# Optimization experiments

Measured on AMD Instinct MI355X. Metric: run time of the kernel, lower is better.

## Reference

```python
import jax, jax.numpy as jnp
import numpy as np

L, N, K, S, V, H = 12, 2048, 8, 4, 50000, 256


def setup_inputs() -> dict:
    key = jax.random.key(0)
    ks = jax.random.split(key, 20)
    tokens1 = jax.random.randint(ks[0], (L, N, S), 0, V, dtype=jnp.int32)
    tokens2 = jax.random.randint(ks[1], (L, N, S), 0, V, dtype=jnp.int32)
    # child indices into previous level's h (0 = zero-init row, -1 = no child)
    idx1 = jax.random.randint(ks[2], (L, N, K), -1, N + 1, dtype=jnp.int32).at[0].set(-1)
    idx2 = jax.random.randint(ks[3], (L, N, K), -1, N + 1, dtype=jnp.int32).at[0].set(-1)
    sc = 0.02
    E = jax.random.normal(ks[4], (V, H), jnp.float32)  # torch.randn init
    lin_W = jax.random.normal(ks[5], (H * S, H), jnp.float32) * sc
    lin_b = jnp.zeros((H,), jnp.float32)
    Uf_W = jax.random.normal(ks[6], (H, H), jnp.float32) * sc
    Uf_b = jnp.zeros((H,), jnp.float32)
    Uiuo_W = jax.random.normal(ks[7], (H, 3 * H), jnp.float32) * sc
    Uiuo_b = jnp.zeros((3 * H,), jnp.float32)
    W_W = jax.random.normal(ks[8], (H, 4 * H), jnp.float32) * sc
    W_b = jnp.zeros((4 * H,), jnp.float32)
    dense_W = jax.random.normal(ks[9], (H, 512), jnp.float32) * sc
    dense_b = jnp.zeros((512,), jnp.float32)
    out_W = jax.random.normal(ks[10], (512, 2), jnp.float32) * sc
    out_b = jnp.zeros((2,), jnp.float32)
    return dict(tokens1=tokens1, idx1=idx1, tokens2=tokens2, idx2=idx2,
                E=E, lin_W=lin_W, lin_b=lin_b, Uf_W=Uf_W, Uf_b=Uf_b,
                Uiuo_W=Uiuo_W, Uiuo_b=Uiuo_b, W_W=W_W, W_b=W_b,
                dense_W=dense_W, dense_b=dense_b, out_W=out_W, out_b=out_b)


def _encode(tokens, idx, E, lin_W, lin_b, Uf_W, Uf_b, Uiuo_W, Uiuo_b, W_W, W_b):
    # TreeEmbeddingLayer: lookup label_size tokens per node, concat, linear
    emb = E[tokens].reshape(L, N, S * H)           # [L,N,S*H]
    x = emb @ lin_W + lin_b                        # [L,N,H]

    def step(carry, inp):
        h_prev, c_prev = carry                     # [N,H]
        xl, il = inp                               # [N,H], [N,K]
        zero = jnp.zeros((1, H), xl.dtype)
        hp = jnp.concatenate([zero, h_prev], 0)    # [N+1,H] (row 0 = init)
        cp = jnp.concatenate([zero, c_prev], 0)
        mask_bool = il != -1
        index = jnp.where(mask_bool, il, 0)
        h = hp[index]                              # [N,K,H] gather child states
        c = cp[index]
        m = mask_bool[..., None].astype(xl.dtype)  # [N,K,1]
        h_sum = jnp.sum(h * m, axis=1)             # [N,H]
        Wx = xl @ W_W + W_b                        # [N,4H]
        Wf, Wi, Wu, Wo = Wx[:, :H], Wx[:, H:2*H], Wx[:, 2*H:3*H], Wx[:, 3*H:]
        fk = jax.nn.sigmoid(Wf[:, None, :] + h @ Uf_W + Uf_b)  # [N,K,H]
        bf = jnp.sum(fk * c * m, axis=1)           # [N,H]
        iuo = h_sum @ Uiuo_W + Uiuo_b              # [N,3H]
        i = jax.nn.sigmoid(iuo[:, :H] + Wi)
        u = jnp.tanh(iuo[:, H:2*H] + Wu)
        o = jax.nn.sigmoid(iuo[:, 2*H:] + Wo)
        nc = i * u + bf
        nh = o * jnp.tanh(nc)
        return (nh, nc), nh

    init = (jnp.zeros((N, H), x.dtype), jnp.zeros((N, H), x.dtype))
    (_, _), hs = jax.lax.scan(step, init, (x, idx))
    # 1 layer with skip connection; hx = last (root) level
    return hs[-1] + x[-1]                          # [N,H]


def reference(tokens1, idx1, tokens2, idx2, E, lin_W, lin_b, Uf_W, Uf_b,
              Uiuo_W, Uiuo_b, W_W, W_b, dense_W, dense_b, out_W, out_b):
    h1 = _encode(tokens1, idx1, E, lin_W, lin_b, Uf_W, Uf_b, Uiuo_W, Uiuo_b, W_W, W_b)
    h2 = _encode(tokens2, idx2, E, lin_W, lin_b, Uf_W, Uf_b, Uiuo_W, Uiuo_b, W_W, W_b)
    abs_dist = jnp.abs(h1 - h2)                    # [N,H]
    x = jnp.tanh(abs_dist @ dense_W + dense_b)     # dropout = identity (eval)
    logits = x @ out_W + out_b                     # [N,2]
    return jax.nn.softmax(logits, axis=-1)
```

## Files before the change

### kernel.cpp

```cpp
#include <hip/hip_runtime.h>

#define LL 12
#define NN 2048
#define KK 8
#define SS 4
#define HH 256
#define LN (LL*NN)
#define VV 50000
#define ZROW 4096
#define SROW 1536

typedef __bf16 bf16_t;
typedef __bf16 bf16x8 __attribute__((ext_vector_type(8)));
typedef __bf16 bf16x4v __attribute__((ext_vector_type(4)));
typedef float f32x4 __attribute__((ext_vector_type(4)));

__device__ __forceinline__ float sigmoidf_(float x) { return 1.f / (1.f + expf(-x)); }

__global__ __launch_bounds__(256) void k_cvtE(const float* __restrict__ src,
                                              bf16_t* __restrict__ dst, int n4)
{
    int i = blockIdx.x * 256 + threadIdx.x;
    const int stride = gridDim.x * 256;
    for (; i < n4; i += stride) {
        const float4 v = ((const float4*)src)[i];
        bf16x4v o;
        o[0] = (bf16_t)v.x; o[1] = (bf16_t)v.y; o[2] = (bf16_t)v.z; o[3] = (bf16_t)v.w;
        ((bf16x4v*)dst)[i] = o;
    }
}

__global__ __launch_bounds__(256) void k_cvtW(
    const float* __restrict__ linW, const float* __restrict__ WW,
    const float* __restrict__ UfW, const float* __restrict__ UiW,
    bf16_t* __restrict__ linWt, bf16_t* __restrict__ WWt,
    bf16_t* __restrict__ UfWt, bf16_t* __restrict__ UiWt)
{
    int i = blockIdx.x * 256 + threadIdx.x;
    if (i < 262144) {
        const int rr = i >> 8, cc = i & 255;
        linWt[(size_t)cc * 1024 + rr] = (bf16_t)linW[i];
        return;
    }
    i -= 262144;
    if (i < 262144) {
        const int rr = i >> 10, cc = i & 1023;
        WWt[(size_t)cc * 256 + rr] = (bf16_t)WW[i];
        return;
    }
    i -= 262144;
    if (i < 65536) {
        const int rr = i >> 8, cc = i & 255;
        UfWt[(size_t)cc * 256 + rr] = (bf16_t)UfW[i];
        return;
    }
    i -= 65536;
    if (i < 196608) {
        const int rr = i / 768, cc = i - rr * 768;
        UiWt[(size_t)cc * 256 + rr] = (bf16_t)UiW[i];
    }
}

__global__ __launch_bounds__(256) void k_zero(float* __restrict__ SA, float* __restrict__ SB)
{
    const int t = threadIdx.x;
    float* a = SA + (size_t)ZROW * 384;
    float* b = SB + (size_t)ZROW * 384;
    for (int i = t; i < 384; i += 256) { a[i] = 0.f; b[i] = 0.f; }
}

__global__ __launch_bounds__(256) void k_embed(
    const int* __restrict__ tok1, const int* __restrict__ tok2,
    const bf16_t* __restrict__ Ebf, const bf16_t* __restrict__ linWt,
    const float* __restrict__ linb, bf16_t* __restrict__ xout)
{
    __shared__ int toff[64][SS];
    const int t = threadIdx.x;
    const int m0 = blockIdx.x * 64;
    {
        const int lr = t >> 2, s = t & 3;
        const int m = m0 + lr;
        const int e = (m >= LN) ? 1 : 0;
        const int rrow = m - e * LN;
        const int* tok = e ? tok2 : tok1;
        toff[lr][s] = tok[(size_t)rrow * SS + s] * HH;
    }
    __syncthreads();
    const int lane = t & 63, w = t >> 6;
    const int wm = w >> 1, wn = w & 1;
    const int r = lane & 15, kg = lane >> 4;
    const int lr0 = wm * 32 + r, lr1 = lr0 + 16;
    const bf16_t* bp[8];
    #pragma unroll
    for (int j = 0; j < 8; ++j)
        bp[j] = linWt + (size_t)(wn * 128 + j * 16 + r) * 1024 + kg * 8;

    const f32x4 zero = {0.f, 0.f, 0.f, 0.f};
    f32x4 acc[2][8];
    #pragma unroll
    for (int mi = 0; mi < 2; ++mi)
        #pragma unroll
        for (int j = 0; j < 8; ++j) acc[mi][j] = zero;

    for (int k0 = 0; k0 < 1024; k0 += 32) {
        const int s = k0 >> 8, off = (k0 & 255) + kg * 8;
        const bf16x8 a0 = *(const bf16x8*)(Ebf + (size_t)toff[lr0][s] + off);
        const bf16x8 a1 = *(const bf16x8*)(Ebf + (size_t)toff[lr1][s] + off);
        #pragma unroll
        for (int j = 0; j < 8; ++j) {
            const bf16x8 b = *(const bf16x8*)bp[j];
            acc[0][j] = __builtin_amdgcn_mfma_f32_16x16x32_bf16(a0, b, acc[0][j], 0, 0, 0);
            acc[1][j] = __builtin_amdgcn_mfma_f32_16x16x32_bf16(a1, b, acc[1][j], 0, 0, 0);
            bp[j] += 32;
        }
    }
    const int crow = m0 + wm * 32 + kg * 4;
    #pragma unroll
    for (int j = 0; j < 8; ++j) {
        const int ccol = wn * 128 + j * 16 + r;
        const float bv = linb[ccol];
        #pragma unroll
        for (int mi = 0; mi < 2; ++mi)
            #pragma unroll
            for (int jj = 0; jj < 4; ++jj)
                xout[(size_t)(crow + mi * 16 + jj) * HH + ccol] =
                    (bf16_t)(acc[mi][j][jj] + bv);
    }
}

__global__ __launch_bounds__(512, 2) void k_step(
    const bf16_t* __restrict__ xbf,
    const int* __restrict__ idx1, const int* __restrict__ idx2, const int l,
    const bf16_t* __restrict__ UfWt, const float* __restrict__ Ufb,
    const bf16_t* __restrict__ UiWt, const float* __restrict__ Uib,
    const bf16_t* __restrict__ WWt, const float* __restrict__ Wb,
    const char* __restrict__ Sprev, char* __restrict__ Snext)
{
    __shared__ __align__(16) bf16_t WxL[16 * 1024];
    __shared__ __align__(16) bf16_t iuoL[16 * 768];
    __shared__ __align__(16) bf16_t hsumL[16 * 256];

    const int t = threadIdx.x;
    const int bid = blockIdx.x;
    const int x  = bid & 7;
    const int e  = x >> 2;
    const int n0 = ((bid >> 3) * 4 + (x & 3)) * 16;
    const int g0 = e * NN + n0;
    const int lane = t & 63, w = t >> 6;
    const int r = lane & 15, kg = lane >> 4;
    const f32x4 zero = {0.f, 0.f, 0.f, 0.f};

    const int rr = t >> 5, sl = t & 31;
    const int ss = (sl + 4 * (rr & 7)) & 31;

    int ch[KK];
    {
        const int* idxp = (e ? idx2 : idx1) + ((size_t)l * NN + n0 + rr) * KK;
        const int4 i0 = *(const int4*)idxp;
        const int4 i1 = *(const int4*)(idxp + 4);
        ch[0] = i0.x; ch[1] = i0.y; ch[2] = i0.z; ch[3] = i0.w;
        ch[4] = i1.x; ch[5] = i1.y; ch[6] = i1.z; ch[7] = i1.w;
        #pragma unroll
        for (int k = 0; k < KK; ++k)
            ch[k] = (ch[k] >= 1) ? (e * NN + ch[k] - 1) : ZROW;
    }

    bf16x8 hv[KK];
    #pragma unroll
    for (int k = 0; k < KK; ++k)
        hv[k] = *(const bf16x8*)(Sprev + (size_t)ch[k] * SROW + sl * 16);

    const bf16_t* xrow = xbf + ((size_t)e * LN + (size_t)l * NN + n0 + r) * HH + kg * 8;
    bf16x8 aWx[8];
    #pragma unroll
    for (int k = 0; k < 8; ++k) aWx[k] = *(const bf16x8*)(xrow + k * 32);

    {
        const bf16_t* bw[8];
        #pragma unroll
        for (int j = 0; j < 8; ++j)
            bw[j] = WWt + (size_t)((8 * w + j) * 16 + r) * HH + kg * 8;
        f32x4 acc[8];
        #pragma unroll
        for (int j = 0; j < 8; ++j) acc[j] = zero;
        #pragma unroll
        for (int k = 0; k < 8; ++k) {
            #pragma unroll
            for (int j = 0; j < 8; ++j) {
                const bf16x8 b = *(const bf16x8*)bw[j];
                acc[j] = __builtin_amdgcn_mfma_f32_16x16x32_bf16(aWx[k], b, acc[j], 0, 0, 0);
                bw[j] += 32;
            }
        }
        #pragma unroll
        for (int j = 0; j < 8; ++j) {
            const int col = (8 * w + j) * 16 + r;
            const float bv = Wb[col];
            #pragma unroll
            for (int jj = 0; jj < 4; ++jj)
                WxL[(size_t)(kg * 4 + jj) * 1024 + col] = (bf16_t)(acc[j][jj] + bv);
        }
    }

    {
        float hs[8] = {0.f, 0.f, 0.f, 0.f, 0.f, 0.f, 0.f, 0.f};
        #pragma unroll
        for (int k = 0; k < KK; ++k) {
            #pragma unroll
            for (int j = 0; j < 8; ++j) hs[j] += (float)hv[k][j];
        }
        bf16x8 o;
        #pragma unroll
        for (int j = 0; j < 8; ++j) o[j] = (bf16_t)hs[j];
        *(bf16x8*)(hsumL + rr * 256 + ss * 8) = o;
    }
    __syncthreads();

    bf16x8 cv[KK], fv[KK];
    #pragma unroll
    for (int k = 0; k < KK; ++k) {
        const char* row = Sprev + (size_t)ch[k] * SROW;
        fv[k] = *(const bf16x8*)(row + 512 + sl * 16);
        cv[k] = *(const bf16x8*)(row + 1024 + sl * 16);
    }

    {
        const bf16_t* bu[6];
        #pragma unroll
        for (int j = 0; j < 6; ++j)
            bu[j] = UiWt + (size_t)((6 * w + j) * 16 + r) * HH + kg * 8;
        f32x4 acc[6];
        #pragma unroll
        for (int j = 0; j < 6; ++j) acc[j] = zero;
        for (int k0 = 0; k0 < HH; k0 += 32) {
            const int sa = (((k0 >> 3) + kg) + 4 * (r & 7)) & 31;
            const bf16x8 a = *(const bf16x8*)(hsumL + r * 256 + sa * 8);
            #pragma unroll
            for (int j = 0; j < 6; ++j) {
                const bf16x8 b = *(const bf16x8*)bu[j];
                acc[j] = __builtin_amdgcn_mfma_f32_16x16x32_bf16(a, b, acc[j], 0, 0, 0);
                bu[j] += 32;
            }
        }
        #pragma unroll
        for (int j = 0; j < 6; ++j) {
            const int col = (6 * w + j) * 16 + r;
            const float bv = Uib[col];
            #pragma unroll
            for (int jj = 0; jj < 4; ++jj)
                iuoL[(size_t)(kg * 4 + jj) * 768 + col] = (bf16_t)(acc[j][jj] + bv);
        }
    }

    float ba[8] = {0.f, 0.f, 0.f, 0.f, 0.f, 0.f, 0.f, 0.f};
    {
        float wf[8];
        const bf16x8 wv = *(const bf16x8*)(WxL + (size_t)rr * 1024 + sl * 8);
        #pragma unroll
        for (int j = 0; j < 8; ++j) wf[j] = (float)wv[j];
        #pragma unroll
        for (int k = 0; k < KK; ++k) {
            #pragma unroll
            for (int j = 0; j < 8; ++j) {
                const float fk = sigmoidf_(wf[j] + (float)fv[k][j]);
                ba[j] = fmaf(fk, (float)cv[k][j], ba[j]);
            }
        }
    }
    __syncthreads();

    {
        const bf16x8 wiv = *(const bf16x8*)(WxL + (size_t)rr * 1024 + 256 + sl * 8);
        const bf16x8 wuv = *(const bf16x8*)(WxL + (size_t)rr * 1024 + 512 + sl * 8);
        const bf16x8 wov = *(const bf16x8*)(WxL + (size_t)rr * 1024 + 768 + sl * 8);
        const bf16x8 iv  = *(const bf16x8*)(iuoL + (size_t)rr * 768 + sl * 8);
        const bf16x8 uv  = *(const bf16x8*)(iuoL + (size_t)rr * 768 + 256 + sl * 8);
        const bf16x8 ov  = *(const bf16x8*)(iuoL + (size_t)rr * 768 + 512 + sl * 8);
        bf16x8 ncb, nhb;
        #pragma unroll
        for (int j = 0; j < 8; ++j) {
            const float ig = sigmoidf_((float)iv[j] + (float)wiv[j]);
            const float ug = tanhf((float)uv[j] + (float)wuv[j]);
            const float og = sigmoidf_((float)ov[j] + (float)wov[j]);
            const float nc = fmaf(ig, ug, ba[j]);
            ncb[j] = (bf16_t)nc;
            nhb[j] = (bf16_t)(og * tanhf(nc));
        }
        char* rowN = Snext + (size_t)(g0 + rr) * SROW;
        *(bf16x8*)(rowN + sl * 16) = nhb;
        *(bf16x8*)(rowN + 1024 + sl * 16) = ncb;
        *(bf16x8*)(hsumL + rr * 256 + ss * 8) = nhb;
    }

    if (l < LL - 1) {
        __syncthreads();
        const int ct0 = 2 * w;
        const bf16_t* bq0 = UfWt + (size_t)(ct0 * 16 + r) * HH + kg * 8;
        const bf16_t* bq1 = bq0 + (size_t)16 * HH;
        f32x4 ac0 = zero, ac1 = zero;
        for (int k0 = 0; k0 < HH; k0 += 32) {
            const int sa = (((k0 >> 3) + kg) + 4 * (r & 7)) & 31;
            const bf16x8 a = *(const bf16x8*)(hsumL + r * 256 + sa * 8);
            const bf16x8 b0 = *(const bf16x8*)bq0;
            const bf16x8 b1 = *(const bf16x8*)bq1;
            ac0 = __builtin_amdgcn_mfma_f32_16x16x32_bf16(a, b0, ac0, 0, 0, 0);
            ac1 = __builtin_amdgcn_mfma_f32_16x16x32_bf16(a, b1, ac1, 0, 0, 0);
            bq0 += 32; bq1 += 32;
        }
        const int c0 = ct0 * 16 + r, c1 = c0 + 16;
        const float bv0 = Ufb[c0], bv1 = Ufb[c1];
        #pragma unroll
        for (int jj = 0; jj < 4; ++jj) {
            bf16_t* fr = (bf16_t*)(Snext + (size_t)(g0 + kg * 4 + jj) * SROW + 512);
            fr[c0] = (bf16_t)(ac0[jj] + bv0);
            fr[c1] = (bf16_t)(ac1[jj] + bv1);
        }
    }
}

__global__ __launch_bounds__(256) void k_final(
    const char* __restrict__ Sfin, const bf16_t* __restrict__ xbf,
    const float* __restrict__ dW, const float* __restrict__ db,
    const float* __restrict__ oW, const float* __restrict__ ob,
    float* __restrict__ out)
{
    __shared__ __align__(16) float ad[8][HH];
    __shared__ __align__(16) float xx[8][512];
    const int t = threadIdx.x;
    const int n0 = blockIdx.x * 8;
    const size_t xoff1 = (size_t)(LL - 1) * NN * HH;
    const size_t xoff2 = (size_t)LN * HH + xoff1;
    #pragma unroll
    for (int rr = 0; rr < 8; ++rr) {
        const int n = n0 + rr;
        const float h1 = (float)((const bf16_t*)(Sfin + (size_t)n * SROW))[t]
                       + (float)xbf[xoff1 + (size_t)n * HH + t];
        const float h2 = (float)((const bf16_t*)(Sfin + (size_t)(NN + n) * SROW))[t]
                       + (float)xbf[xoff2 + (size_t)n * HH + t];
        ad[rr][t] = fabsf(h1 - h2);
    }
    __syncthreads();
    float a0[8], a1[8];
    #pragma unroll
    for (int rr = 0; rr < 8; ++rr) { a0[rr] = 0.f; a1[rr] = 0.f; }
    for (int k = 0; k < HH; k += 4) {
        #pragma unroll
        for (int kk = 0; kk < 4; ++kk) {
            const float b0 = dW[(size_t)(k + kk) * 512 + t];
            const float b1 = dW[(size_t)(k + kk) * 512 + 256 + t];
            #pragma unroll
            for (int rr = 0; rr < 8; ++rr) {
                const float av = ad[rr][k + kk];
                a0[rr] = fmaf(av, b0, a0[rr]);
                a1[rr] = fmaf(av, b1, a1[rr]);
            }
        }
    }
    const float db0 = db[t], db1 = db[256 + t];
    #pragma unroll
    for (int rr = 0; rr < 8; ++rr) {
        xx[rr][t] = tanhf(a0[rr] + db0);
        xx[rr][256 + t] = tanhf(a1[rr] + db1);
    }
    __syncthreads();
    const int w = t >> 6, lane = t & 63;
    for (int rr = w; rr < 8; rr += 4) {
        float p0 = 0.f, p1 = 0.f;
        for (int k = lane; k < 512; k += 64) {
            const float xv = xx[rr][k];
            p0 = fmaf(xv, oW[2 * k + 0], p0);
            p1 = fmaf(xv, oW[2 * k + 1], p1);
        }
        #pragma unroll
        for (int off = 32; off > 0; off >>= 1) {
            p0 += __shfl_down(p0, off);
            p1 += __shfl_down(p1, off);
        }
        if (lane == 0) {
            const float l0 = p0 + ob[0], l1 = p1 + ob[1];
            const float mx = fmaxf(l0, l1);
            const float e0 = expf(l0 - mx), e1 = expf(l1 - mx);
            const float inv = 1.f / (e0 + e1);
            out[(size_t)(n0 + rr) * 2 + 0] = e0 * inv;
            out[(size_t)(n0 + rr) * 2 + 1] = e1 * inv;
        }
    }
}

extern "C" void kernel_launch(void* const* d_in, const int* in_sizes, int n_in,
                              void* d_out, int out_size, void* d_ws, size_t ws_size,
                              hipStream_t stream) {
    (void)in_sizes; (void)n_in; (void)out_size; (void)ws_size;
    const int*   tok1 = (const int*)d_in[0];
    const int*   idx1 = (const int*)d_in[1];
    const int*   tok2 = (const int*)d_in[2];
    const int*   idx2 = (const int*)d_in[3];
    const float* E    = (const float*)d_in[4];
    const float* linW = (const float*)d_in[5];
    const float* linb = (const float*)d_in[6];
    const float* UfW  = (const float*)d_in[7];
    const float* Ufb  = (const float*)d_in[8];
    const float* UiW  = (const float*)d_in[9];
    const float* Uib  = (const float*)d_in[10];
    const float* WW   = (const float*)d_in[11];
    const float* Wb   = (const float*)d_in[12];
    const float* dW   = (const float*)d_in[13];
    const float* db   = (const float*)d_in[14];
    const float* oW   = (const float*)d_in[15];
    const float* ob   = (const float*)d_in[16];
    float* out = (float*)d_out;

    bf16_t* xbf = (bf16_t*)d_ws;
    char*   uni = (char*)(xbf + (size_t)12582912);
    bf16_t* Ebf = (bf16_t*)uni;
    char*   SA  = uni;
    char*   SB  = uni + 6292992;
    bf16_t* linWt = (bf16_t*)(uni + 25600000);
    bf16_t* WWt   = linWt + (size_t)262144;
    bf16_t* UfWt  = WWt   + (size_t)262144;
    bf16_t* UiWt  = UfWt  + (size_t)65536;

    k_cvtE<<<2048, 256, 0, stream>>>(E, Ebf, VV * HH / 4);
    k_cvtW<<<3072, 256, 0, stream>>>(linW, WW, UfW, UiW, linWt, WWt, UfWt, UiWt);

    k_embed<<<768, 256, 0, stream>>>(tok1, tok2, Ebf, linWt, linb, xbf);

    k_zero<<<1, 256, 0, stream>>>((float*)SA, (float*)SB);

    char *Sp = SA, *Sn = SB;
    for (int l = 0; l < LL; ++l) {
        k_step<<<256, 512, 0, stream>>>(xbf, idx1, idx2, l,
                                        UfWt, Ufb, UiWt, Uib, WWt, Wb, Sp, Sn);
        char* ts = Sp; Sp = Sn; Sn = ts;
    }

    k_final<<<NN / 8, 256, 0, stream>>>(Sp, xbf, dW, db, oW, ob, out);
}
```

Before: 701.6 us.

## Precompute next level's W·x in step kernel, off the critical path

A new kernel computes level 0's x@W projection ahead of time. Each step kernel then computes the W·x projection for the next level after finishing its own work and writes it to a double-buffered global array. The current level reads its projection from global memory instead of running the MFMA GEMM at the start, and all child h/f/c gathers are issued together up front. The aim is to shorten the dependent chain at the start of each step so gathers overlap better. The cost is extra global traffic for the Wx buffers, roughly 8 MB per level, plus an extra kernel launch.

```diff
diff --git a/kernel.cpp b/kernel.cpp
--- a/kernel.cpp
+++ b/kernel.cpp
@@ -128,15 +128,67 @@
     }
 }
 
-__global__ __launch_bounds__(512, 2) void k_step(
+__global__ __launch_bounds__(256) void k_wx0(
+    const bf16_t* __restrict__ xbf, const bf16_t* __restrict__ WWt,
+    const float* __restrict__ Wb, bf16_t* __restrict__ Wx0)
+{
+    const int n0 = blockIdx.x * 256;
+    const int m0 = blockIdx.y * 64;
+    const int t = threadIdx.x;
+    const int lane = t & 63, w = t >> 6;
+    const int wm = w >> 1, wn = w & 1;
+    const int r = lane & 15, kg = lane >> 4;
+    const int e = (m0 >= NN) ? 1 : 0;
+    const size_t xb = (size_t)e * LN + (m0 - e * NN);
+    const int lr0 = wm * 32 + r, lr1 = lr0 + 16;
+    const bf16_t* ap0 = xbf + (xb + lr0) * HH + kg * 8;
+    const bf16_t* ap1 = xbf + (xb + lr1) * HH + kg * 8;
+    const bf16_t* bp[8];
+    #pragma unroll
+    for (int j = 0; j < 8; ++j)
+        bp[j] = WWt + (size_t)(n0 + wn * 128 + j * 16 + r) * HH + kg * 8;
+
+    const f32x4 zero = {0.f, 0.f, 0.f, 0.f};
+    f32x4 acc[2][8];
+    #pragma unroll
+    for (int mi = 0; mi < 2; ++mi)
+        #pragma unroll
+        for (int j = 0; j < 8; ++j) acc[mi][j] = zero;
+
+    for (int k0 = 0; k0 < HH; k0 += 32) {
+        const bf16x8 a0 = *(const bf16x8*)(ap0 + k0);
+        const bf16x8 a1 = *(const bf16x8*)(ap1 + k0);
+        #pragma unroll
+        for (int j = 0; j < 8; ++j) {
+            const bf16x8 b = *(const bf16x8*)bp[j];
+            acc[0][j] = __builtin_amdgcn_mfma_f32_16x16x32_bf16(a0, b, acc[0][j], 0, 0, 0);
+            acc[1][j] = __builtin_amdgcn_mfma_f32_16x16x32_bf16(a1, b, acc[1][j], 0, 0, 0);
+            bp[j] += 32;
+        }
+    }
+    const int crow = m0 + wm * 32 + kg * 4;
+    #pragma unroll
+    for (int j = 0; j < 8; ++j) {
+        const int ccol = n0 + wn * 128 + j * 16 + r;
+        const float bv = Wb[ccol];
+        #pragma unroll
+        for (int mi = 0; mi < 2; ++mi)
+            #pragma unroll
+            for (int jj = 0; jj < 4; ++jj)
+                Wx0[(size_t)(crow + mi * 16 + jj) * 1024 + ccol] =
+                    (bf16_t)(acc[mi][j][jj] + bv);
+    }
+}
+
+__global__ __launch_bounds__(512, 2) void k_step3(
     const bf16_t* __restrict__ xbf,
     const int* __restrict__ idx1, const int* __restrict__ idx2, const int l,
     const bf16_t* __restrict__ UfWt, const float* __restrict__ Ufb,
     const bf16_t* __restrict__ UiWt, const float* __restrict__ Uib,
     const bf16_t* __restrict__ WWt, const float* __restrict__ Wb,
+    const bf16_t* __restrict__ WxCur, bf16_t* __restrict__ WxNext,
     const char* __restrict__ Sprev, char* __restrict__ Snext)
 {
-    __shared__ __align__(16) bf16_t WxL[16 * 1024];
     __shared__ __align__(16) bf16_t iuoL[16 * 768];
     __shared__ __align__(16) bf16_t hsumL[16 * 256];
 
@@ -165,41 +217,23 @@
             ch[k] = (ch[k] >= 1) ? (e * NN + ch[k] - 1) : ZROW;
     }
 
-    bf16x8 hv[KK];
-    #pragma unroll
-    for (int k = 0; k < KK; ++k)
-        hv[k] = *(const bf16x8*)(Sprev + (size_t)ch[k] * SROW + sl * 16);
-
-    const bf16_t* xrow = xbf + ((size_t)e * LN + (size_t)l * NN + n0 + r) * HH + kg * 8;
+    const bf16_t* wxp = WxCur + (size_t)(g0 + rr) * 1024;
+    const bf16x8 wfv = *(const bf16x8*)(wxp + sl * 8);
+    const bf16x8 wiv = *(const bf16x8*)(wxp + 256 + sl * 8);
+    const bf16x8 wuv = *(const bf16x8*)(wxp + 512 + sl * 8);
+    const bf16x8 wov = *(const bf16x8*)(wxp + 768 + sl * 8);
+    const int lx = (l < LL - 1) ? (l + 1) : l;
+    const bf16_t* xrow = xbf + ((size_t)e * LN + (size_t)lx * NN + n0 + r) * HH + kg * 8;
     bf16x8 aWx[8];
     #pragma unroll
     for (int k = 0; k < 8; ++k) aWx[k] = *(const bf16x8*)(xrow + k * 32);
-
-    {
-        const bf16_t* bw[8];
-        #pragma unroll
-        for (int j = 0; j < 8; ++j)
-            bw[j] = WWt + (size_t)((8 * w + j) * 16 + r) * HH + kg * 8;
-        f32x4 acc[8];
-        #pragma unroll
-        for (int j = 0; j < 8; ++j) acc[j] = zero;
-        #pragma unroll
-        for (int k = 0; k < 8; ++k) {
-            #pragma unroll
-            for (int j = 0; j < 8; ++j) {
-                const bf16x8 b = *(const bf16x8*)bw[j];
-                acc[j] = __builtin_amdgcn_mfma_f32_16x16x32_bf16(aWx[k], b, acc[j], 0, 0, 0);
-                bw[j] += 32;
-            }
-        }
-        #pragma unroll
-        for (int j = 0; j < 8; ++j) {
-            const int col = (8 * w + j) * 16 + r;
-            const float bv = Wb[col];
-            #pragma unroll
-            for (int jj = 0; jj < 4; ++jj)
-                WxL[(size_t)(kg * 4 + jj) * 1024 + col] = (bf16_t)(acc[j][jj] + bv);
-        }
+    bf16x8 hv[KK], fv[KK], cv[KK];
+    #pragma unroll
+    for (int k = 0; k < KK; ++k) {
+        const char* row = Sprev + (size_t)ch[k] * SROW;
+        hv[k] = *(const bf16x8*)(row + sl * 16);
+        fv[k] = *(const bf16x8*)(row + 512 + sl * 16);
+        cv[k] = *(const bf16x8*)(row + 1024 + sl * 16);
     }
 
     {
@@ -215,14 +249,6 @@
         *(bf16x8*)(hsumL + rr * 256 + ss * 8) = o;
     }
     __syncthreads();
-
-    bf16x8 cv[KK], fv[KK];
-    #pragma unroll
-    for (int k = 0; k < KK; ++k) {
-        const char* row = Sprev + (size_t)ch[k] * SROW;
-        fv[k] = *(const bf16x8*)(row + 512 + sl * 16);
-        cv[k] = *(const bf16x8*)(row + 1024 + sl * 16);
-    }
 
     {
         const bf16_t* bu[6];
@@ -255,9 +281,8 @@
     float ba[8] = {0.f, 0.f, 0.f, 0.f, 0.f, 0.f, 0.f, 0.f};
     {
         float wf[8];
-        const bf16x8 wv = *(const bf16x8*)(WxL + (size_t)rr * 1024 + sl * 8);
-        #pragma unroll
-        for (int j = 0; j < 8; ++j) wf[j] = (float)wv[j];
+        #pragma unroll
+        for (int j = 0; j < 8; ++j) wf[j] = (float)wfv[j];
         #pragma unroll
         for (int k = 0; k < KK; ++k) {
             #pragma unroll
@@ -270,12 +295,9 @@
     __syncthreads();
 
     {
-        const bf16x8 wiv = *(const bf16x8*)(WxL + (size_t)rr * 1024 + 256 + sl * 8);
-        const bf16x8 wuv = *(const bf16x8*)(WxL + (size_t)rr * 1024 + 512 + sl * 8);
-        const bf16x8 wov = *(const bf16x8*)(WxL + (size_t)rr * 1024 + 768 + sl * 8);
-        const bf16x8 iv  = *(const bf16x8*)(iuoL + (size_t)rr * 768 + sl * 8);
-        const bf16x8 uv  = *(const bf16x8*)(iuoL + (size_t)rr * 768 + 256 + sl * 8);
-        const bf16x8 ov  = *(const bf16x8*)(iuoL + (size_t)rr * 768 + 512 + sl * 8);
+        const bf16x8 iv = *(const bf16x8*)(iuoL + (size_t)rr * 768 + sl * 8);
+        const bf16x8 uv = *(const bf16x8*)(iuoL + (size_t)rr * 768 + 256 + sl * 8);
+        const bf16x8 ov = *(const bf16x8*)(iuoL + (size_t)rr * 768 + 512 + sl * 8);
         bf16x8 ncb, nhb;
         #pragma unroll
         for (int j = 0; j < 8; ++j) {
@@ -294,26 +316,55 @@
 
     if (l < LL - 1) {
         __syncthreads();
-        const int ct0 = 2 * w;
-        const bf16_t* bq0 = UfWt + (size_t)(ct0 * 16 + r) * HH + kg * 8;
-        const bf16_t* bq1 = bq0 + (size_t)16 * HH;
-        f32x4 ac0 = zero, ac1 = zero;
-        for (int k0 = 0; k0 < HH; k0 += 32) {
-            const int sa = (((k0 >> 3) + kg) + 4 * (r & 7)) & 31;
-            const bf16x8 a = *(const bf16x8*)(hsumL + r * 256 + sa * 8);
-            const bf16x8 b0 = *(const bf16x8*)bq0;
-            const bf16x8 b1 = *(const bf16x8*)bq1;
-            ac0 = __builtin_amdgcn_mfma_f32_16x16x32_bf16(a, b0, ac0, 0, 0, 0);
-            ac1 = __builtin_amdgcn_mfma_f32_16x16x32_bf16(a, b1, ac1, 0, 0, 0);
-            bq0 += 32; bq1 += 32;
-        }
-        const int c0 = ct0 * 16 + r, c1 = c0 + 16;
-        const float bv0 = Ufb[c0], bv1 = Ufb[c1];
-        #pragma unroll
-        for (int jj = 0; jj < 4; ++jj) {
-            bf16_t* fr = (bf16_t*)(Snext + (size_t)(g0 + kg * 4 + jj) * SROW + 512);
-            fr[c0] = (bf16_t)(ac0[jj] + bv0);
-            fr[c1] = (bf16_t)(ac1[jj] + bv1);
+        {
+            const int ct0 = 2 * w;
+            const bf16_t* bq0 = UfWt + (size_t)(ct0 * 16 + r) * HH + kg * 8;
+            const bf16_t* bq1 = bq0 + (size_t)16 * HH;
+            f32x4 ac0 = zero, ac1 = zero;
+            for (int k0 = 0; k0 < HH; k0 += 32) {
+                const int sa = (((k0 >> 3) + kg) + 4 * (r & 7)) & 31;
+                const bf16x8 a = *(const bf16x8*)(hsumL + r * 256 + sa * 8);
+                const bf16x8 b0 = *(const bf16x8*)bq0;
+                const bf16x8 b1 = *(const bf16x8*)bq1;
+                ac0 = __builtin_amdgcn_mfma_f32_16x16x32_bf16(a, b0, ac0, 0, 0, 0);
+                ac1 = __builtin_amdgcn_mfma_f32_16x16x32_bf16(a, b1, ac1, 0, 0, 0);
+                bq0 += 32; bq1 += 32;
+            }
+            const int c0 = ct0 * 16 + r, c1 = c0 + 16;
+            const float bv0 = Ufb[c0], bv1 = Ufb[c1];
+            #pragma unroll
+            for (int jj = 0; jj < 4; ++jj) {
+                bf16_t* fr = (bf16_t*)(Snext + (size_t)(g0 + kg * 4 + jj) * SROW + 512);
+                fr[c0] = (bf16_t)(ac0[jj] + bv0);
+                fr[c1] = (bf16_t)(ac1[jj] + bv1);
+            }
+        }
+        {
+            const bf16_t* bw[8];
+            #pragma unroll
+            for (int j = 0; j < 8; ++j)
+                bw[j] = WWt + (size_t)((8 * w + j) * 16 + r) * HH + kg * 8;
+            f32x4 acc[8];
+            #pragma unroll
+            for (int j = 0; j < 8; ++j) acc[j] = zero;
+            #pragma unroll
+            for (int k = 0; k < 8; ++k) {
+                #pragma unroll
+                for (int j = 0; j < 8; ++j) {
+                    const bf16x8 b = *(const bf16x8*)bw[j];
+                    acc[j] = __builtin_amdgcn_mfma_f32_16x16x32_bf16(aWx[k], b, acc[j], 0, 0, 0);
+                    bw[j] += 32;
+                }
+            }
+            #pragma unroll
+            for (int j = 0; j < 8; ++j) {
+                const int col = (8 * w + j) * 16 + r;
+                const float bv = Wb[col];
+                #pragma unroll
+                for (int jj = 0; jj < 4; ++jj)
+                    WxNext[(size_t)(g0 + kg * 4 + jj) * 1024 + col] =
+                        (bf16_t)(acc[j][jj] + bv);
+            }
         }
     }
 }
@@ -411,11 +462,14 @@
     float* out = (float*)d_out;
 
     bf16_t* xbf = (bf16_t*)d_ws;
-    char*   uni = (char*)(xbf + (size_t)12582912);
+    char*   uni = (char*)d_ws + 25165824;
     bf16_t* Ebf = (bf16_t*)uni;
     char*   SA  = uni;
     char*   SB  = uni + 6292992;
-    bf16_t* linWt = (bf16_t*)(uni + 25600000);
+    bf16_t* WxA = (bf16_t*)(uni + 12585984);
+    bf16_t* WxB = (bf16_t*)(uni + 12585984 + 8388608);
+    char*   wts = uni + 12585984 + 2 * 8388608;
+    bf16_t* linWt = (bf16_t*)wts;
     bf16_t* WWt   = linWt + (size_t)262144;
     bf16_t* UfWt  = WWt   + (size_t)262144;
     bf16_t* UiWt  = UfWt  + (size_t)65536;
@@ -424,14 +478,17 @@
     k_cvtW<<<3072, 256, 0, stream>>>(linW, WW, UfW, UiW, linWt, WWt, UfWt, UiWt);
 
     k_embed<<<768, 256, 0, stream>>>(tok1, tok2, Ebf, linWt, linb, xbf);
-
+    k_wx0<<<dim3(4, 64), 256, 0, stream>>>(xbf, WWt, Wb, WxA);
     k_zero<<<1, 256, 0, stream>>>((float*)SA, (float*)SB);
 
     char *Sp = SA, *Sn = SB;
+    bf16_t *Wc = WxA, *Wn = WxB;
     for (int l = 0; l < LL; ++l) {
-        k_step<<<256, 512, 0, stream>>>(xbf, idx1, idx2, l,
-                                        UfWt, Ufb, UiWt, Uib, WWt, Wb, Sp, Sn);
+        k_step3<<<256, 512, 0, stream>>>(xbf, idx1, idx2, l,
+                                         UfWt, Ufb, UiWt, Uib, WWt, Wb,
+                                         Wc, Wn, Sp, Sn);
         char* ts = Sp; Sp = Sn; Sn = ts;
+        bf16_t* tw = Wc; Wc = Wn; Wn = tw;
     }
 
     k_final<<<NN / 8, 256, 0, stream>>>(Sp, xbf, dW, db, oW, ob, out);
```

New measurement: 731.1 us. 4.2% more time.
